# Performance work log

Measured on AMD Instinct MI355X. Metric: run time of the kernel, lower is better.

## Reference

```python
import jax, jax.numpy as jnp
import numpy as np

B, S, E, G, O, TOPK = 4, 2048, 1024, 8, 4096, 2


def setup_inputs() -> dict:
    key = jax.random.key(0)
    k1, k2, k3, k4 = jax.random.split(key, 4)
    return {
        "hidden_states": jax.random.normal(k1, (B, S, E), dtype=jnp.float32),
        "WG": jax.random.normal(k2, (E, G), dtype=jnp.float32) * (1.0 / np.sqrt(E)),
        "Wi": jax.random.normal(k3, (G, E, O), dtype=jnp.float32) * (1.0 / np.sqrt(E)),
        "down": jax.random.normal(k4, (O, E), dtype=jnp.float32) * (1.0 / np.sqrt(O)),
        "topk": TOPK,
    }


def reference(hidden_states, WG, Wi, down, topk):
    # gate logits: [b, s, g]
    gate = jnp.matmul(hidden_states, WG)
    # sparse path (smoe_fwd): topk mask zeroes non-selected gate LOGITS,
    # so non-selected experts get sigmoid(0) = 0.5 (faithful to source).
    _, idx = jax.lax.top_k(gate, topk)              # [b, s, topk]
    mask = jnp.max(jax.nn.one_hot(idx, gate.shape[-1], dtype=gate.dtype), axis=-2)  # [b, s, g]
    w = jax.nn.sigmoid(gate * mask)                  # [b, s, g]
    # weighted combination over all expert matrices: [b, s, o]
    y = jnp.einsum('bse,bsg,geo->bso', hidden_states, w, Wi)
    # squared ReLU
    h = jnp.square(jax.nn.relu(y))
    return jnp.matmul(h, down)                       # [b, s, e]
```

## Files before the change

### kernel.cpp

```cpp
#include <hip/hip_runtime.h>
#include <hip/hip_bf16.h>
#include <math.h>

typedef __bf16 bf16;
typedef __bf16 bf16x4 __attribute__((ext_vector_type(4)));
typedef __bf16 bf16x8 __attribute__((ext_vector_type(8)));
typedef float  floatx4 __attribute__((ext_vector_type(4)));

#define N_TOK 8192
#define E_DIM 1024
#define G_DIM 8
#define O_DIM 4096
#define EPI_LD 132

__device__ __forceinline__ void gload_lds16(const void* g, void* l) {
    __builtin_amdgcn_global_load_lds(
        (__attribute__((address_space(1))) void*)(g),
        (__attribute__((address_space(3))) void*)(l),
        16, 0, 0);
}

__global__ __launch_bounds__(256) void gate_compute(
    const float* __restrict__ X,
    const float* __restrict__ WG,
    int* __restrict__ sel,
    float* __restrict__ sval)
{
    __shared__ float lwgT[G_DIM * E_DIM];
    const int tid  = threadIdx.x;
    const int wave = tid >> 6;
    const int lane = tid & 63;

#pragma unroll
    for (int k = 0; k < 8; ++k) {
        const int i = k * 256 + tid;
        const float4 v = *(const float4*)(WG + i * 4);
        const int e  = i >> 1;
        const int g0 = (i & 1) * 4;
        lwgT[(g0 + 0) * E_DIM + e] = v.x;
        lwgT[(g0 + 1) * E_DIM + e] = v.y;
        lwgT[(g0 + 2) * E_DIM + e] = v.z;
        lwgT[(g0 + 3) * E_DIM + e] = v.w;
    }
    __syncthreads();

    const int t = blockIdx.x * 4 + wave;
    float acc[G_DIM];
#pragma unroll
    for (int g = 0; g < G_DIM; ++g) acc[g] = 0.f;

#pragma unroll
    for (int it = 0; it < 4; ++it) {
        const int e0 = it * 256 + lane * 4;
        const float4 xv = *(const float4*)(X + (long)t * E_DIM + e0);
#pragma unroll
        for (int g = 0; g < G_DIM; ++g) {
            const float4 wv = *(const float4*)(lwgT + g * E_DIM + e0);
            acc[g] += xv.x * wv.x + xv.y * wv.y + xv.z * wv.z + xv.w * wv.w;
        }
    }
#pragma unroll
    for (int g = 0; g < G_DIM; ++g) {
        float v = acc[g];
#pragma unroll
        for (int off = 32; off > 0; off >>= 1) v += __shfl_down(v, off, 64);
        acc[g] = v;
    }
    if (lane == 0) {
        int i1 = 0;
#pragma unroll
        for (int g = 1; g < G_DIM; ++g) if (acc[g] > acc[i1]) i1 = g;
        int i2 = (i1 == 0) ? 1 : 0;
#pragma unroll
        for (int g = 0; g < G_DIM; ++g)
            if (g != i1 && g != i2 && acc[g] > acc[i2]) i2 = g;
#pragma unroll
        for (int s = 0; s < 2; ++s) {
            const int g = s ? i2 : i1;
            sel[t * 2 + s]  = g;
            sval[t * 2 + s] = 1.f / (1.f + expf(-acc[g])) - 0.5f;
        }
    }
}

__global__ __launch_bounds__(1024) void route_kernel(
    const int* __restrict__ sel, const float* __restrict__ sval,
    int* __restrict__ cnt, int* __restrict__ off, int* __restrict__ offp,
    int* __restrict__ tok, float* __restrict__ scl, int* __restrict__ pos)
{
    __shared__ int hcnt[16][G_DIM];
    __shared__ int wbase[16][G_DIM];
    const int tid  = threadIdx.x;
    const int w    = tid >> 6;
    const int lane = tid & 63;
    const unsigned long long below = ((unsigned long long)1 << lane) - 1;

    int c0[G_DIM];
#pragma unroll
    for (int g = 0; g < G_DIM; ++g) c0[g] = 0;
    for (int c = 0; c < 16; ++c) {
        const int g = sel[w * 1024 + c * 64 + lane];
#pragma unroll
        for (int gg = 0; gg < G_DIM; ++gg)
            c0[gg] += __popcll(__ballot(g == gg));
    }
    if (lane == 0)
#pragma unroll
        for (int g = 0; g < G_DIM; ++g) hcnt[w][g] = c0[g];
    __syncthreads();

    if (tid == 0) {
        int tot[G_DIM];
#pragma unroll
        for (int g = 0; g < G_DIM; ++g) {
            int a = 0;
            for (int ww = 0; ww < 16; ++ww) { wbase[ww][g] = a; a += hcnt[ww][g]; }
            tot[g] = a; cnt[g] = a;
        }
        int a = 0, b = 0;
#pragma unroll
        for (int g = 0; g < G_DIM; ++g) {
            off[g]  = a; a += tot[g];
            offp[g] = b; b += (tot[g] + 127) & ~127;
        }
        offp[G_DIM] = b;
    }
    __syncthreads();

    int run[G_DIM];
#pragma unroll
    for (int g = 0; g < G_DIM; ++g) run[g] = 0;
    for (int c = 0; c < 16; ++c) {
        const int idx = w * 1024 + c * 64 + lane;
        const int g   = sel[idx];
        const float sv = sval[idx];
        int myrank = 0;
#pragma unroll
        for (int gg = 0; gg < G_DIM; ++gg) {
            const unsigned long long m = __ballot(g == gg);
            const int r = run[gg] + __popcll(m & below);
            if (g == gg) myrank = r;
            run[gg] += __popcll(m);
        }
        const int p = wbase[w][g] + myrank;
        tok[g * N_TOK + p] = idx >> 1;
        scl[g * N_TOK + p] = sv;
        pos[idx] = (g << 16) | p;
    }
}

__global__ __launch_bounds__(256) void convert_x(
    const float* __restrict__ X, bf16* __restrict__ Xb)
{
    const long i = ((long)blockIdx.x * 256 + threadIdx.x) * 4;
    const float4 v = *(const float4*)(X + i);
    bf16x4 o;
    o[0] = (bf16)v.x; o[1] = (bf16)v.y; o[2] = (bf16)v.z; o[3] = (bf16)v.w;
    *(bf16x4*)(Xb + i) = o;
}

__global__ __launch_bounds__(256) void transpose_conv(
    const float* __restrict__ S, bf16* __restrict__ D, int R, int C)
{
    __shared__ float tile[64][65];
    const int r0  = blockIdx.x * 64;
    const int c0  = blockIdx.y * 64;
    const int tid = threadIdx.x;
    const int tr  = tid >> 4;
    const int tc4 = (tid & 15) * 4;

#pragma unroll
    for (int p = 0; p < 4; ++p) {
        const int r = p * 16 + tr;
        const float4 v = *(const float4*)(S + (long)(r0 + r) * C + c0 + tc4);
        tile[r][tc4 + 0] = v.x;
        tile[r][tc4 + 1] = v.y;
        tile[r][tc4 + 2] = v.z;
        tile[r][tc4 + 3] = v.w;
    }
    __syncthreads();
#pragma unroll
    for (int p = 0; p < 4; ++p) {
        const int c = p * 16 + tr;
        bf16x4 o;
        o[0] = (bf16)tile[tc4 + 0][c];
        o[1] = (bf16)tile[tc4 + 1][c];
        o[2] = (bf16)tile[tc4 + 2][c];
        o[3] = (bf16)tile[tc4 + 3][c];
        *(bf16x4*)(D + (long)(c0 + c) * R + r0 + tc4) = o;
    }
}

__global__ __launch_bounds__(256) void wsum_kernel(
    const bf16* __restrict__ WiT, bf16* __restrict__ WsumT)
{
    const int o  = blockIdx.x;
    const int e4 = threadIdx.x * 4;
    float a0 = 0.f, a1 = 0.f, a2 = 0.f, a3 = 0.f;
#pragma unroll
    for (int g = 0; g < G_DIM; ++g) {
        const bf16x4 v = *(const bf16x4*)(WiT + (long)o * 8192 + g * E_DIM + e4);
        a0 += (float)v[0]; a1 += (float)v[1]; a2 += (float)v[2]; a3 += (float)v[3];
    }
    bf16x4 w;
    w[0] = (bf16)(0.5f * a0); w[1] = (bf16)(0.5f * a1);
    w[2] = (bf16)(0.5f * a2); w[3] = (bf16)(0.5f * a3);
    *(bf16x4*)(WsumT + (long)o * E_DIM + e4) = w;
}

__global__ __launch_bounds__(128) void gather_rows(
    const bf16* __restrict__ Xb, const int* __restrict__ cnt,
    const int* __restrict__ offp, const int* __restrict__ tok,
    bf16* __restrict__ Xs)
{
    const int slot = blockIdx.x;
    if (slot >= offp[G_DIM]) return;
    int g = 0;
    while (slot >= offp[g + 1]) ++g;
    const int p = slot - offp[g];
    bf16* dst = Xs + (long)slot * E_DIM + threadIdx.x * 8;
    if (p < cnt[g]) {
        const bf16* src = Xb + (long)tok[g * N_TOK + p] * E_DIM + threadIdx.x * 8;
        *(bf16x8*)dst = *(const bf16x8*)src;
    } else {
        bf16x8 z = {};
        *(bf16x8*)dst = z;
    }
}

__device__ __forceinline__ void gemm_core256(
    const bf16* __restrict__ Ap, long lda,
    const bf16* __restrict__ Bp, long ldb,
    int K, char* smem, floatx4 (&acc)[8][4])
{
    const int tid  = threadIdx.x;
    const int wave = tid >> 6;
    const int lane = tid & 63;
    const int wm   = wave >> 2;
    const int wn   = wave & 3;
    const int fr   = lane & 15;
    const int fq   = lane >> 4;

#pragma unroll
    for (int i = 0; i < 8; ++i)
#pragma unroll
        for (int j = 0; j < 4; ++j)
            acc[i][j] = (floatx4){0.f, 0.f, 0.f, 0.f};

    const int  srow = tid >> 3;
    const int  ssw  = ((tid & 7) * 16) ^ ((srow & 7) << 4);
    const char* sa  = (const char*)Ap + (long)srow * (lda * 2) + ssw;
    const char* sb  = (const char*)Bp + (long)srow * (ldb * 2) + ssw;
    const long a64  = lda * 128;
    const long b64  = ldb * 128;
    char* const lw  = smem + wave * 1024;

#define STAGE256(buf, kt) do {                                              \
        const long _ko = (long)(kt) * 128;                                  \
        char* _lb = lw + (buf) * 65536;                                     \
        _Pragma("unroll")                                                   \
        for (int _c = 0; _c < 4; ++_c) {                                    \
            gload_lds16(sa + _ko + _c * a64, _lb + _c * 8192);              \
            gload_lds16(sb + _ko + _c * b64, _lb + 32768 + _c * 8192);      \
        }                                                                   \
    } while (0)

    const int xsw  = (fr & 7) << 4;
    const int ko0  = (fq * 16) ^ xsw;
    const int ko1  = (fq * 16 + 64) ^ xsw;
    const int aoff = (wm * 128 + fr) * 128;
    const int boff = 32768 + (wn * 64 + fr) * 128;

    const int nt = K >> 6;
    STAGE256(0, 0);
    STAGE256(1, 1);
    asm volatile("s_waitcnt vmcnt(8)" ::: "memory");
    __builtin_amdgcn_s_barrier();
    __builtin_amdgcn_sched_barrier(0);

    bf16x8 af[4][2], bv[2][2];

    for (int t = 0; t < nt; ++t) {
        const char* base = smem + ((t & 1) << 16);

#pragma unroll
        for (int i = 0; i < 4; ++i) {
            af[i][0] = *(const bf16x8*)(base + aoff + i * 2048 + ko0);
            af[i][1] = *(const bf16x8*)(base + aoff + i * 2048 + ko1);
        }
#pragma unroll
        for (int j = 0; j < 2; ++j) {
            bv[j][0] = *(const bf16x8*)(base + boff + j * 2048 + ko0);
            bv[j][1] = *(const bf16x8*)(base + boff + j * 2048 + ko1);
        }
        __builtin_amdgcn_s_setprio(1);
#pragma unroll
        for (int i = 0; i < 4; ++i)
#pragma unroll
            for (int j = 0; j < 2; ++j) {
                acc[i][j] = __builtin_amdgcn_mfma_f32_16x16x32_bf16(af[i][0], bv[j][0], acc[i][j], 0, 0, 0);
                acc[i][j] = __builtin_amdgcn_mfma_f32_16x16x32_bf16(af[i][1], bv[j][1], acc[i][j], 0, 0, 0);
            }
        __builtin_amdgcn_s_setprio(0);

#pragma unroll
        for (int j = 0; j < 2; ++j) {
            bv[j][0] = *(const bf16x8*)(base + boff + 4096 + j * 2048 + ko0);
            bv[j][1] = *(const bf16x8*)(base + boff + 4096 + j * 2048 + ko1);
        }
        __builtin_amdgcn_s_setprio(1);
#pragma unroll
        for (int i = 0; i < 4; ++i)
#pragma unroll
            for (int j = 0; j < 2; ++j) {
                acc[i][2 + j] = __builtin_amdgcn_mfma_f32_16x16x32_bf16(af[i][0], bv[j][0], acc[i][2 + j], 0, 0, 0);
                acc[i][2 + j] = __builtin_amdgcn_mfma_f32_16x16x32_bf16(af[i][1], bv[j][1], acc[i][2 + j], 0, 0, 0);
            }
        __builtin_amdgcn_s_setprio(0);

#pragma unroll
        for (int i = 0; i < 4; ++i) {
            af[i][0] = *(const bf16x8*)(base + aoff + 8192 + i * 2048 + ko0);
            af[i][1] = *(const bf16x8*)(base + aoff + 8192 + i * 2048 + ko1);
        }
        __builtin_amdgcn_s_setprio(1);
#pragma unroll
        for (int i = 0; i < 4; ++i)
#pragma unroll
            for (int j = 0; j < 2; ++j) {
                acc[4 + i][2 + j] = __builtin_amdgcn_mfma_f32_16x16x32_bf16(af[i][0], bv[j][0], acc[4 + i][2 + j], 0, 0, 0);
                acc[4 + i][2 + j] = __builtin_amdgcn_mfma_f32_16x16x32_bf16(af[i][1], bv[j][1], acc[4 + i][2 + j], 0, 0, 0);
            }
        __builtin_amdgcn_s_setprio(0);

#pragma unroll
        for (int j = 0; j < 2; ++j) {
            bv[j][0] = *(const bf16x8*)(base + boff + j * 2048 + ko0);
            bv[j][1] = *(const bf16x8*)(base + boff + j * 2048 + ko1);
        }
        __builtin_amdgcn_s_setprio(1);
#pragma unroll
        for (int i = 0; i < 4; ++i)
#pragma unroll
            for (int j = 0; j < 2; ++j) {
                acc[4 + i][j] = __builtin_amdgcn_mfma_f32_16x16x32_bf16(af[i][0], bv[j][0], acc[4 + i][j], 0, 0, 0);
                acc[4 + i][j] = __builtin_amdgcn_mfma_f32_16x16x32_bf16(af[i][1], bv[j][1], acc[4 + i][j], 0, 0, 0);
            }
        __builtin_amdgcn_s_setprio(0);

        __builtin_amdgcn_sched_barrier(0);
        __builtin_amdgcn_s_barrier();
        if (t + 2 < nt) {
            STAGE256(t & 1, t + 2);
            asm volatile("s_waitcnt vmcnt(8)" ::: "memory");
        } else {
            asm volatile("s_waitcnt vmcnt(0)" ::: "memory");
        }
        __builtin_amdgcn_s_barrier();
        __builtin_amdgcn_sched_barrier(0);
    }
#undef STAGE256
}

__global__ __launch_bounds__(512, 2) void gemm256_base(
    const bf16* __restrict__ A, const bf16* __restrict__ BT,
    bf16* __restrict__ C)
{
    __shared__ __align__(16) char smem[131072];
    const int u   = blockIdx.x;
    const int xcd = u & 7;
    const int s   = u >> 3;
    const int mt  = s & 31;
    const int ct  = xcd + 8 * (s >> 5);
    const int row0 = mt * 256, col0 = ct * 256;

    floatx4 acc[8][4];
    gemm_core256(A + (long)row0 * E_DIM, E_DIM,
                 BT + (long)col0 * E_DIM, E_DIM,
                 E_DIM, smem, acc);

    const int tid = threadIdx.x, wave = tid >> 6, lane = tid & 63;
    const int wm = wave >> 2, wn = wave & 3, fr = lane & 15, fq = lane >> 4;
    bf16* tile = (bf16*)smem;
#pragma unroll
    for (int i = 0; i < 8; ++i)
#pragma unroll
        for (int j = 0; j < 4; ++j)
#pragma unroll
            for (int r = 0; r < 4; ++r)
                tile[(wm * 128 + i * 16 + fq * 4 + r) * 256 + wn * 64 + j * 16 + fr] =
                    (bf16)(acc[i][j][r]);
    __syncthreads();
#pragma unroll
    for (int k = 0; k < 16; ++k) {
        const int rl = (tid >> 5) + k * 16;
        const int cc = (tid & 31) * 8;
        *(bf16x8*)(C + (long)(row0 + rl) * O_DIM + col0 + cc) =
            *(const bf16x8*)(tile + rl * 256 + cc);
    }
}

__global__ __launch_bounds__(512, 2) void gemm256_sparse(
    const bf16* __restrict__ Xs,
    const bf16* __restrict__ WiT,
    const int* __restrict__ cnt,
    const int* __restrict__ off,
    const int* __restrict__ offp,
    const float* __restrict__ scl,
    bf16* __restrict__ ysp)
{
    const int u   = blockIdx.x;
    const int xcd = u & 7;
    const int s   = u >> 3;
    const int mt  = s & 63;
    const int pc  = xcd + 8 * (s >> 6);
    const int g   = pc & 7;
    const int ct  = pc >> 3;

    const int cg     = cnt[g];
    const int base_p = offp[g];
    const int cgp    = offp[g + 1] - base_p;
    const int m0     = mt * 256;
    if (m0 >= cgp) return;

    __shared__ __align__(16) char smem[131072];
    const int col0 = ct * 256;

    floatx4 acc[8][4];
    gemm_core256(Xs + (long)(base_p + m0) * E_DIM, E_DIM,
                 WiT + (long)col0 * 8192 + g * E_DIM, 8192,
                 E_DIM, smem, acc);

    const int tid = threadIdx.x, wave = tid >> 6, lane = tid & 63;
    const int wm = wave >> 2, wn = wave & 3, fr = lane & 15, fq = lane >> 4;
    const float* sclg = scl + g * N_TOK;
    const int clmax = cg - 1;
    bf16* tile = (bf16*)smem;
#pragma unroll
    for (int i = 0; i < 8; ++i)
#pragma unroll
        for (int r = 0; r < 4; ++r) {
            const int rl = wm * 128 + i * 16 + fq * 4 + r;
            const int gm = m0 + rl;
            const float sv = sclg[gm > clmax ? clmax : gm];
#pragma unroll
            for (int j = 0; j < 4; ++j)
                tile[rl * 256 + wn * 64 + j * 16 + fr] = (bf16)(sv * acc[i][j][r]);
        }
    __syncthreads();
    const long ob = off[g] + m0;
#pragma unroll
    for (int k = 0; k < 16; ++k) {
        const int rl = (tid >> 5) + k * 16;
        if (m0 + rl < cg) {
            const int cc = (tid & 31) * 8;
            *(bf16x8*)(ysp + (ob + rl) * O_DIM + col0 + cc) =
                *(const bf16x8*)(tile + rl * 256 + cc);
        }
    }
}

template <typename OUT, bool VEC>
__global__ __launch_bounds__(256, 4) void gemm_mt(
    const bf16* __restrict__ A, int lda,
    const bf16* __restrict__ BT, int ldb,
    OUT* __restrict__ C, int ldc, int K)
{
    __shared__ char smem[VEC ? (128 * EPI_LD * 2) : 16384];
    bf16* As = (bf16*)smem;
    bf16* Bs = (bf16*)(smem + 8192);

    const int u   = blockIdx.x;
    const int xcd = u & 7;
    const int s   = u >> 3;
    const int mt  = s & 63;
    const int col = xcd + 8 * (s >> 6);

    const int tid  = threadIdx.x;
    const int wave = tid >> 6;
    const int lane = tid & 63;
    const int row0 = mt * 128;
    const int col0 = col * 128;

    const int sr = lane >> 2;
    const int sc = (lane & 3) * 8;
    const bf16* agp0 = A  + (long)(row0 + 16 * wave       + sr) * lda + sc;
    const bf16* agp1 = A  + (long)(row0 + 16 * (wave + 4) + sr) * lda + sc;
    const bf16* bgp0 = BT + (long)(col0 + 16 * wave       + sr) * ldb + sc;
    const bf16* bgp1 = BT + (long)(col0 + 16 * (wave + 4) + sr) * ldb + sc;
    bf16* asl0 = As + (long)wave * 512;
    bf16* asl1 = As + (long)(wave + 4) * 512;
    bf16* bsl0 = Bs + (long)wave * 512;
    bf16* bsl1 = Bs + (long)(wave + 4) * 512;

    const int mi_base = (wave >> 1) * 64;
    const int ni_base = (wave & 1) * 64;
    const int fr = lane & 15;
    const int fq = lane >> 4;

    floatx4 acc[4][4] = {};

    for (int k0 = 0; k0 < K; k0 += 32) {
        __syncthreads();
        gload_lds16(agp0 + k0, (void*)asl0);
        gload_lds16(agp1 + k0, (void*)asl1);
        gload_lds16(bgp0 + k0, (void*)bsl0);
        gload_lds16(bgp1 + k0, (void*)bsl1);
        __syncthreads();

        bf16x8 af[4], bfr[4];
#pragma unroll
        for (int i = 0; i < 4; ++i) {
            af[i]  = *(const bf16x8*)(As + (mi_base + i * 16 + fr) * 32 + fq * 8);
            bfr[i] = *(const bf16x8*)(Bs + (ni_base + i * 16 + fr) * 32 + fq * 8);
        }
#pragma unroll
        for (int i = 0; i < 4; ++i)
#pragma unroll
            for (int j = 0; j < 4; ++j)
                acc[i][j] = __builtin_amdgcn_mfma_f32_16x16x32_bf16(
                    af[i], bfr[j], acc[i][j], 0, 0, 0);
    }

    if (VEC) {
        __syncthreads();
        bf16* tile = (bf16*)smem;
#pragma unroll
        for (int i = 0; i < 4; ++i)
#pragma unroll
            for (int j = 0; j < 4; ++j)
#pragma unroll
                for (int r = 0; r < 4; ++r) {
                    const int rl = mi_base + i * 16 + fq * 4 + r;
                    const int cl = ni_base + j * 16 + fr;
                    tile[rl * EPI_LD + cl] = (bf16)acc[i][j][r];
                }
        __syncthreads();
#pragma unroll
        for (int k = 0; k < 8; ++k) {
            const int rl = (tid >> 3) + 32 * (k >> 1);
            const int cl = (tid & 7) * 8 + 64 * (k & 1);
            const bf16x8 v = *(const bf16x8*)(tile + rl * EPI_LD + cl);
            *(bf16x8*)((bf16*)C + (long)(row0 + rl) * ldc + col0 + cl) = v;
        }
    } else {
#pragma unroll
        for (int i = 0; i < 4; ++i)
#pragma unroll
            for (int j = 0; j < 4; ++j)
#pragma unroll
                for (int r = 0; r < 4; ++r) {
                    const long row = row0 + mi_base + i * 16 + fq * 4 + r;
                    const long cg  = col0 + ni_base + j * 16 + fr;
                    C[row * ldc + cg] = (OUT)acc[i][j][r];
                }
    }
}

__global__ __launch_bounds__(256) void relu2_gather(
    const bf16* __restrict__ Yb,
    const bf16* __restrict__ ysp,
    const int* __restrict__ pos,
    const int* __restrict__ off,
    bf16* __restrict__ H)
{
    const int t  = blockIdx.x;
    const int p0 = pos[t * 2];
    const int p1 = pos[t * 2 + 1];
    const long r0 = off[p0 >> 16] + (p0 & 0xffff);
    const long r1 = off[p1 >> 16] + (p1 & 0xffff);
    const int c = threadIdx.x * 16;

    const bf16* yb = Yb + (long)t * O_DIM + c;
    const bf16* s0 = ysp + r0 * O_DIM + c;
    const bf16* s1 = ysp + r1 * O_DIM + c;
    bf16* hp = H + (long)t * O_DIM + c;

#pragma unroll
    for (int h = 0; h < 2; ++h) {
        const bf16x8 a = *(const bf16x8*)(yb + h * 8);
        const bf16x8 b = *(const bf16x8*)(s0 + h * 8);
        const bf16x8 d = *(const bf16x8*)(s1 + h * 8);
        bf16x8 o;
#pragma unroll
        for (int k = 0; k < 8; ++k) {
            float v = (float)a[k] + (float)b[k] + (float)d[k];
            v = fmaxf(v, 0.f);
            o[k] = (bf16)(v * v);
        }
        *(bf16x8*)(hp + h * 8) = o;
    }
}

extern "C" void kernel_launch(void* const* d_in, const int* in_sizes, int n_in,
                              void* d_out, int out_size, void* d_ws, size_t ws_size,
                              hipStream_t stream)
{
    const float* X  = (const float*)d_in[0];
    const float* WG = (const float*)d_in[1];
    const float* Wi = (const float*)d_in[2];
    const float* dn = (const float*)d_in[3];
    float* out = (float*)d_out;

    char* ws = (char*)d_ws;
    const long MB = 1l << 20;
    int*   cnt   = (int*)ws;
    int*   off   = (int*)(ws + 1024);
    int*   offp  = (int*)(ws + 2048);
    int*   pos   = (int*)(ws + 4096);
    int*   tok   = (int*)(ws + 128 * 1024);
    float* scl   = (float*)(ws + 448 * 1024);
    int*   sel   = (int*)(ws + 704 * 1024);
    float* sval  = (float*)(ws + 768 * 1024);
    bf16*  dnT   = (bf16*)(ws + 1 * MB);
    bf16*  WiT   = (bf16*)(ws + 9 * MB);
    bf16*  Hh    = (bf16*)(ws + 9 * MB);
    bf16*  Xs    = (bf16*)(ws + 73 * MB);
    bf16*  Yb    = (bf16*)(ws + 107 * MB);
    bf16*  ysp   = (bf16*)(ws + 171 * MB);
    bf16*  Xb    = (bf16*)(ws + 171 * MB);
    bf16*  WsumT = (bf16*)(ws + 187 * MB);

    gate_compute<<<dim3(N_TOK / 4), dim3(256), 0, stream>>>(X, WG, sel, sval);
    route_kernel<<<dim3(1), dim3(1024), 0, stream>>>(sel, sval, cnt, off, offp,
                                                     tok, scl, pos);
    convert_x<<<dim3(N_TOK * E_DIM / 1024), dim3(256), 0, stream>>>(X, Xb);
    transpose_conv<<<dim3(8192 / 64, O_DIM / 64), dim3(256), 0, stream>>>(Wi, WiT, 8192, O_DIM);
    transpose_conv<<<dim3(O_DIM / 64, E_DIM / 64), dim3(256), 0, stream>>>(dn, dnT, O_DIM, E_DIM);
    wsum_kernel<<<dim3(O_DIM), dim3(256), 0, stream>>>(WiT, WsumT);
    gemm256_base<<<dim3(512), dim3(512), 0, stream>>>(Xb, WsumT, Yb);
    gather_rows<<<dim3(17408), dim3(128), 0, stream>>>(Xb, cnt, offp, tok, Xs);
    gemm256_sparse<<<dim3(8192), dim3(512), 0, stream>>>(
        Xs, WiT, cnt, off, offp, scl, ysp);
    relu2_gather<<<dim3(N_TOK), dim3(256), 0, stream>>>(Yb, ysp, pos, off, Hh);
    gemm_mt<float, false><<<dim3(64 * 8), dim3(256), 0, stream>>>(
        Hh, O_DIM, dnT, O_DIM, out, E_DIM, O_DIM);
}
```

Measured before the change: 742.4 us.

## Restructure 256x256 GEMM core into four-phase interleaved load/MFMA pipeline

Splits each 64-wide K tile into two 32-wide halves stored as separate 64-byte-row LDS subtiles with a new XOR swizzle. Global-to-LDS loads for the next tiles are issued piecemeal across four compute phases rather than as one bulk stage after a barrier. This is meant to hide memory latency and cut the end-of-iteration stall. The cost is more barriers per iteration, and the last iterations redundantly reload a clamped K tile.

Result: faster. 720.2 us (-3.0%).

```diff
diff --git a/kernel.cpp b/kernel.cpp
--- a/kernel.cpp
+++ b/kernel.cpp
@@ -247,119 +247,133 @@
         for (int j = 0; j < 4; ++j)
             acc[i][j] = (floatx4){0.f, 0.f, 0.f, 0.f};
 
-    const int  srow = tid >> 3;
-    const int  ssw  = ((tid & 7) * 16) ^ ((srow & 7) << 4);
-    const char* sa  = (const char*)Ap + (long)srow * (lda * 2) + ssw;
-    const char* sb  = (const char*)Bp + (long)srow * (ldb * 2) + ssw;
-    const long a64  = lda * 128;
-    const long b64  = ldb * 128;
-    char* const lw  = smem + wave * 1024;
-
-#define STAGE256(buf, kt) do {                                              \
-        const long _ko = (long)(kt) * 128;                                  \
-        char* _lb = lw + (buf) * 65536;                                     \
-        _Pragma("unroll")                                                   \
-        for (int _c = 0; _c < 4; ++_c) {                                    \
-            gload_lds16(sa + _ko + _c * a64, _lb + _c * 8192);              \
-            gload_lds16(sb + _ko + _c * b64, _lb + 32768 + _c * 8192);      \
-        }                                                                   \
+    const int  srow = tid >> 2;
+    const int  ksw  = (((tid & 3) ^ ((tid >> 3) & 3)) << 4);
+    const char* sa  = (const char*)Ap + (long)srow * (lda * 2) + ksw;
+    const char* sb  = (const char*)Bp + (long)srow * (ldb * 2) + ksw;
+    const long aR   = lda * 256;
+    const long bR   = ldb * 256;
+    const int  ldsW = wave * 1024;
+
+#define STAGE_H(sbase, src, rstr, kb) do {                                   \
+        gload_lds16((src) + (kb),          smem + (sbase) + ldsW);           \
+        gload_lds16((src) + (kb) + (rstr), smem + (sbase) + 8192 + ldsW);    \
     } while (0)
 
-    const int xsw  = (fr & 7) << 4;
-    const int ko0  = (fq * 16) ^ xsw;
-    const int ko1  = (fq * 16 + 64) ^ xsw;
-    const int aoff = (wm * 128 + fr) * 128;
-    const int boff = 32768 + (wn * 64 + fr) * 128;
+    const int asw = ((fq ^ ((fr >> 1) & 3)) << 4);
+    const int aro = (wm * 128 + fr) * 64 + asw;
+    const int bro = (wn * 64 + fr) * 64 + asw;
 
     const int nt = K >> 6;
-    STAGE256(0, 0);
-    STAGE256(1, 1);
-    asm volatile("s_waitcnt vmcnt(8)" ::: "memory");
+
+    {
+        const long k1 = (nt > 1) ? 128 : 0;
+        STAGE_H(0,             sa, aR, 0);
+        STAGE_H(32768,         sb, bR, 0);
+        STAGE_H(16384,         sa, aR, 64);
+        STAGE_H(49152,         sb, bR, 64);
+        STAGE_H(65536 + 32768, sb, bR, k1);
+        STAGE_H(65536 + 0,     sa, aR, k1);
+    }
+    asm volatile("s_waitcnt vmcnt(4)" ::: "memory");
     __builtin_amdgcn_s_barrier();
     __builtin_amdgcn_sched_barrier(0);
 
-    bf16x8 af[4][2], bv[2][2];
+#define LD8(v, off) (v) = *(const bf16x8*)(smem + (off))
+#define PHASE_MID() do {                                                     \
+        __builtin_amdgcn_sched_barrier(0);                                   \
+        __builtin_amdgcn_s_barrier();                                        \
+        asm volatile("s_waitcnt lgkmcnt(0)" ::: "memory");                   \
+        __builtin_amdgcn_sched_barrier(0);                                   \
+    } while (0)
+#define PHASE_END() do {                                                     \
+        __builtin_amdgcn_sched_barrier(0);                                   \
+        __builtin_amdgcn_s_barrier();                                        \
+        __builtin_amdgcn_sched_barrier(0);                                   \
+    } while (0)
+#define PHASE_END_V() do {                                                   \
+        __builtin_amdgcn_sched_barrier(0);                                   \
+        asm volatile("s_waitcnt vmcnt(8)" ::: "memory");                     \
+        __builtin_amdgcn_s_barrier();                                        \
+        __builtin_amdgcn_sched_barrier(0);                                   \
+    } while (0)
+
+    bf16x8 af[4], bq[4];
 
     for (int t = 0; t < nt; ++t) {
-        const char* base = smem + ((t & 1) << 16);
-
-#pragma unroll
-        for (int i = 0; i < 4; ++i) {
-            af[i][0] = *(const bf16x8*)(base + aoff + i * 2048 + ko0);
-            af[i][1] = *(const bf16x8*)(base + aoff + i * 2048 + ko1);
-        }
-#pragma unroll
-        for (int j = 0; j < 2; ++j) {
-            bv[j][0] = *(const bf16x8*)(base + boff + j * 2048 + ko0);
-            bv[j][1] = *(const bf16x8*)(base + boff + j * 2048 + ko1);
-        }
+        const int  bo  = (t & 1) << 16;
+        const int  nbo = bo ^ 65536;
+        const long k1  = (long)((t + 1 < nt) ? t + 1 : nt - 1) * 128;
+        const long k2  = (long)((t + 2 < nt) ? t + 2 : nt - 1) * 128;
+
+#pragma unroll
+        for (int i = 0; i < 4; ++i) LD8(af[i], bo + aro + i * 1024);
+#pragma unroll
+        for (int j = 0; j < 4; ++j) LD8(bq[j], bo + 32768 + bro + j * 1024);
+        STAGE_H(nbo + 49152, sb, bR, k1 + 64);
+        PHASE_MID();
         __builtin_amdgcn_s_setprio(1);
 #pragma unroll
         for (int i = 0; i < 4; ++i)
 #pragma unroll
-            for (int j = 0; j < 2; ++j) {
-                acc[i][j] = __builtin_amdgcn_mfma_f32_16x16x32_bf16(af[i][0], bv[j][0], acc[i][j], 0, 0, 0);
-                acc[i][j] = __builtin_amdgcn_mfma_f32_16x16x32_bf16(af[i][1], bv[j][1], acc[i][j], 0, 0, 0);
-            }
+            for (int j = 0; j < 4; ++j)
+                acc[i][j] = __builtin_amdgcn_mfma_f32_16x16x32_bf16(
+                    af[i], bq[j], acc[i][j], 0, 0, 0);
         __builtin_amdgcn_s_setprio(0);
-
-#pragma unroll
-        for (int j = 0; j < 2; ++j) {
-            bv[j][0] = *(const bf16x8*)(base + boff + 4096 + j * 2048 + ko0);
-            bv[j][1] = *(const bf16x8*)(base + boff + 4096 + j * 2048 + ko1);
-        }
+        PHASE_END();
+
+#pragma unroll
+        for (int i = 0; i < 4; ++i) LD8(af[i], bo + aro + 4096 + i * 1024);
+        STAGE_H(nbo + 16384, sa, aR, k1 + 64);
+        PHASE_MID();
         __builtin_amdgcn_s_setprio(1);
 #pragma unroll
         for (int i = 0; i < 4; ++i)
 #pragma unroll
-            for (int j = 0; j < 2; ++j) {
-                acc[i][2 + j] = __builtin_amdgcn_mfma_f32_16x16x32_bf16(af[i][0], bv[j][0], acc[i][2 + j], 0, 0, 0);
-                acc[i][2 + j] = __builtin_amdgcn_mfma_f32_16x16x32_bf16(af[i][1], bv[j][1], acc[i][2 + j], 0, 0, 0);
-            }
+            for (int j = 0; j < 4; ++j)
+                acc[4 + i][j] = __builtin_amdgcn_mfma_f32_16x16x32_bf16(
+                    af[i], bq[j], acc[4 + i][j], 0, 0, 0);
         __builtin_amdgcn_s_setprio(0);
-
-#pragma unroll
-        for (int i = 0; i < 4; ++i) {
-            af[i][0] = *(const bf16x8*)(base + aoff + 8192 + i * 2048 + ko0);
-            af[i][1] = *(const bf16x8*)(base + aoff + 8192 + i * 2048 + ko1);
-        }
+        PHASE_END_V();
+
+#pragma unroll
+        for (int i = 0; i < 4; ++i) LD8(af[i], bo + 16384 + aro + i * 1024);
+#pragma unroll
+        for (int j = 0; j < 4; ++j) LD8(bq[j], bo + 49152 + bro + j * 1024);
+        STAGE_H(bo + 32768, sb, bR, k2);
+        PHASE_MID();
         __builtin_amdgcn_s_setprio(1);
 #pragma unroll
         for (int i = 0; i < 4; ++i)
 #pragma unroll
-            for (int j = 0; j < 2; ++j) {
-                acc[4 + i][2 + j] = __builtin_amdgcn_mfma_f32_16x16x32_bf16(af[i][0], bv[j][0], acc[4 + i][2 + j], 0, 0, 0);
-                acc[4 + i][2 + j] = __builtin_amdgcn_mfma_f32_16x16x32_bf16(af[i][1], bv[j][1], acc[4 + i][2 + j], 0, 0, 0);
-            }
+            for (int j = 0; j < 4; ++j)
+                acc[i][j] = __builtin_amdgcn_mfma_f32_16x16x32_bf16(
+                    af[i], bq[j], acc[i][j], 0, 0, 0);
         __builtin_amdgcn_s_setprio(0);
-
-#pragma unroll
-        for (int j = 0; j < 2; ++j) {
-            bv[j][0] = *(const bf16x8*)(base + boff + j * 2048 + ko0);
-            bv[j][1] = *(const bf16x8*)(base + boff + j * 2048 + ko1);
-        }
+        PHASE_END();
+
+#pragma unroll
+        for (int i = 0; i < 4; ++i) LD8(af[i], bo + 16384 + aro + 4096 + i * 1024);
+        STAGE_H(bo + 0, sa, aR, k2);
+        PHASE_MID();
         __builtin_amdgcn_s_setprio(1);
 #pragma unroll
         for (int i = 0; i < 4; ++i)
 #pragma unroll
-            for (int j = 0; j < 2; ++j) {
-                acc[4 + i][j] = __builtin_amdgcn_mfma_f32_16x16x32_bf16(af[i][0], bv[j][0], acc[4 + i][j], 0, 0, 0);
-                acc[4 + i][j] = __builtin_amdgcn_mfma_f32_16x16x32_bf16(af[i][1], bv[j][1], acc[4 + i][j], 0, 0, 0);
-            }
+            for (int j = 0; j < 4; ++j)
+                acc[4 + i][j] = __builtin_amdgcn_mfma_f32_16x16x32_bf16(
+                    af[i], bq[j], acc[4 + i][j], 0, 0, 0);
         __builtin_amdgcn_s_setprio(0);
-
-        __builtin_amdgcn_sched_barrier(0);
-        __builtin_amdgcn_s_barrier();
-        if (t + 2 < nt) {
-            STAGE256(t & 1, t + 2);
-            asm volatile("s_waitcnt vmcnt(8)" ::: "memory");
-        } else {
-            asm volatile("s_waitcnt vmcnt(0)" ::: "memory");
-        }
-        __builtin_amdgcn_s_barrier();
-        __builtin_amdgcn_sched_barrier(0);
-    }
-#undef STAGE256
+        PHASE_END_V();
+    }
+
+    asm volatile("s_waitcnt vmcnt(0)" ::: "memory");
+    __builtin_amdgcn_s_barrier();
+#undef STAGE_H
+#undef LD8
+#undef PHASE_MID
+#undef PHASE_END
+#undef PHASE_END_V
 }
 
 __global__ __launch_bounds__(512, 2) void gemm256_base(
```
